# Performance work log

Measured on AMD Instinct MI355X. Metric: run time of the kernel, lower is better.

Reference implementation:

```python
import jax, jax.numpy as jnp
import numpy as np

D_MODEL = 256; N_LEVELS = 4; N_HEADS = 8; N_POINTS = 4
H_SP = 32; W_SP = 32
B = 2; LEN_Q = 1024; LEN_IN = N_LEVELS * H_SP * W_SP
D_HEAD = D_MODEL // N_HEADS
K9 = 9 * N_POINTS  # 3x3 neighborhood around each of the top-k matches


def setup_inputs() -> dict:
    key = jax.random.key(0)
    k1, k2, k3, k4 = jax.random.split(key, 4)
    bound = (6.0 / (D_MODEL + D_MODEL)) ** 0.5  # xavier_uniform for output_proj
    return {
        "query": jax.random.normal(k1, (B, LEN_Q, D_MODEL), jnp.float32),
        "reference_points": jax.random.uniform(k2, (B, LEN_Q, N_LEVELS, 2), dtype=jnp.float32),
        "input_flatten": jax.random.normal(k3, (B, LEN_IN, D_MODEL), jnp.float32),
        # all levels share the same h==w==32 spatial shape (required by the module)
        "input_spatial_shapes": np.full((N_LEVELS, 2), H_SP, dtype=np.int64),
        "input_level_start_index": (np.arange(N_LEVELS) * H_SP * W_SP).astype(np.int64),
        "out_proj_w": jax.random.uniform(k4, (D_MODEL, D_MODEL), jnp.float32, -bound, bound),
        "out_proj_b": jnp.zeros((D_MODEL,), jnp.float32),
    }


def _sample_offset(query, input_flatten, h, w, t):
    # per-head correlation -> softmax -> top-k index -> 3x3 neighborhood -> (x,y) offsets
    n, lq, _ = query.shape
    q = query.reshape(n, lq, N_HEADS, D_HEAD)
    v = input_flatten.reshape(n, -1, N_HEADS, D_HEAD)
    corr = jnp.einsum('nqhd,nkhd->nhqk', q, v) / D_HEAD          # [n,H,lq,Lin]
    corr = corr.reshape(n, N_HEADS, lq, t, h * w)
    prob = jax.nn.softmax(10.0 * corr, axis=-1)
    _, idx = jax.lax.top_k(prob, N_POINTS)                        # [n,H,lq,t,P] int32
    deltas = jnp.array([-1 - h, -h, 1 - h, -1, 0, 1, -1 + h, h, 1 + h], jnp.int32)
    # torch cat order is delta-major: all P points for delta1, then delta2, ...
    res = (idx[..., None, :] + deltas[:, None]).reshape(n, N_HEADS, lq, t, K9)
    res = jnp.clip(res, 0, (h - 1) * (w - 1))                     # faithful (h-1)*(w-1) clamp
    resf = res.astype(jnp.float32)
    off_w = jnp.floor(resf / h)
    off_h = resf - off_w * h
    offsets = jnp.stack([off_w, off_h], axis=-1)                  # [n,H,lq,t,K9,2]
    return jnp.transpose(offsets, (0, 2, 1, 3, 4, 5))             # [n,lq,H,L,K9,2]


def _ms_deform_attn(value, loc, h, w):
    # value [n,Lin,H,dh]; loc in [0,1], [n,lq,H,L,K9,2]; grid_sample-style bilinear, zero pad
    n, lq = loc.shape[0], loc.shape[1]
    v = value.reshape(n, N_LEVELS, h * w, N_HEADS, D_HEAD)
    v = jnp.transpose(v, (0, 3, 1, 2, 4))                         # [n,H,L,hw,dh]
    x = loc[..., 0] * w - 0.5
    y = loc[..., 1] * h - 0.5
    x0 = jnp.floor(x); y0 = jnp.floor(y)
    lw = x - x0; lh = y - y0
    attn_w = 1.0 / (N_LEVELS * K9)  # softmax of all-ones buffer is uniform
    acc = jnp.zeros((n, lq, N_HEADS, D_HEAD), jnp.float32)
    corners = ((y0, x0, (1 - lh) * (1 - lw)), (y0, x0 + 1, (1 - lh) * lw),
               (y0 + 1, x0, lh * (1 - lw)), (y0 + 1, x0 + 1, lh * lw))
    for yi, xi, wgt in corners:
        valid = (yi >= 0) & (yi < h) & (xi >= 0) & (xi < w)
        ii = (jnp.clip(yi, 0, h - 1) * w + jnp.clip(xi, 0, w - 1)).astype(jnp.int32)
        ww = jnp.where(valid, wgt, 0.0) * attn_w                  # [n,lq,H,L,K9]
        ii_t = jnp.transpose(ii, (0, 2, 3, 1, 4)).reshape(n, N_HEADS, N_LEVELS, lq * K9)
        g = jnp.take_along_axis(v, ii_t[..., None], axis=3)       # [n,H,L,lq*K9,dh]
        g = g.reshape(n, N_HEADS, N_LEVELS, lq, K9, D_HEAD)
        ww_t = jnp.transpose(ww, (0, 2, 3, 1, 4))                 # [n,H,L,lq,K9]
        acc = acc + jnp.einsum('nhlqk,nhlqkd->nqhd', ww_t, g)
    return acc.reshape(n, lq, D_MODEL)


def reference(query, reference_points, input_flatten, input_spatial_shapes,
              input_level_start_index, out_proj_w, out_proj_b):
    ss = np.asarray(input_spatial_shapes)
    h = int(ss[0, 0]); w = h
    lin = input_flatten.shape[1]
    t = lin // (h * w)  # == N_LEVELS
    value = input_flatten.reshape(input_flatten.shape[0], lin, N_HEADS, D_HEAD)
    offsets = _sample_offset(query, input_flatten, h, w, t)
    assert reference_points.shape[-1] == 2
    normalizer = jnp.asarray(np.stack([ss[:, 1], ss[:, 0]], -1), jnp.float32)  # [L,2]=(w,h)
    loc = offsets / normalizer[None, None, None, :, None, :]
    out = _ms_deform_attn(value, loc, h, w)
    out = out @ out_proj_w.T + out_proj_b
    return out, loc
```

## Files before the change

kernel.cpp:

```cpp
#include <hip/hip_runtime.h>
#include <math.h>

#define BB 2
#define LQ 1024
#define DM 256
#define NH 8
#define DH 32
#define NL 4
#define HWsp 1024
#define LIN 4096
#define K9 36
#define NGRP (BB * NH * NL * LQ)

typedef short bf16x8 __attribute__((ext_vector_type(8)));
typedef float f32x4 __attribute__((ext_vector_type(4)));

__device__ __forceinline__ ushort bf16rn(float x) {
  unsigned u = __float_as_uint(x);
  unsigned r = (u + 0x7FFFu + ((u >> 16) & 1u)) >> 16;
  return (ushort)r;
}
__device__ __forceinline__ float bf16tof(ushort h) {
  return __uint_as_float(((unsigned)h) << 16);
}

#define INSERT4(val, index)                                              \
  {                                                                      \
    const float v_ = (val);                                              \
    const int ix_ = (index);                                             \
    if (v_ > v3) {                                                       \
      if (v_ > v1) {                                                     \
        if (v_ > v0) {                                                   \
          v3 = v2; i3 = i2; v2 = v1; i2 = i1; v1 = v0; i1 = i0;          \
          v0 = v_; i0 = ix_;                                             \
        } else {                                                         \
          v3 = v2; i3 = i2; v2 = v1; i2 = i1; v1 = v_; i1 = ix_;         \
        }                                                                \
      } else {                                                           \
        if (v_ > v2) {                                                   \
          v3 = v2; i3 = i2; v2 = v_; i2 = ix_;                           \
        } else {                                                         \
          v3 = v_; i3 = ix_;                                             \
        }                                                                \
      }                                                                  \
    }                                                                    \
  }

#define LMAX(av, ai, bv, bi)                                        \
  {                                                                 \
    const bool g_ = ((av) > (bv)) || ((av) == (bv) && (ai) < (bi)); \
    if (!g_) { (av) = (bv); (ai) = (bi); }                          \
  }
#define CEX(av, ai, bv, bi)                                         \
  {                                                                 \
    const bool g_ = ((av) > (bv)) || ((av) == (bv) && (ai) < (bi)); \
    const float tv_ = g_ ? (av) : (bv);                             \
    const int ti_ = g_ ? (ai) : (bi);                               \
    (bv) = g_ ? (bv) : (av); (bi) = g_ ? (bi) : (ai);               \
    (av) = tv_; (ai) = ti_;                                         \
  }

#define PSTRIDE ((size_t)BB * NL * NH * 1024 * 32)

__global__ __launch_bounds__(256) void vsplit_kernel(
    const float* __restrict__ value, ushort* __restrict__ vs) {
  const int T = blockIdx.x * 256 + threadIdx.x;
  const int flat = T << 3;
  const int n = flat >> 20;
  const int rem = flat & 0xFFFFF;
  const int lin = rem >> 8;
  const int d0 = rem & 255;
  const int l = lin >> 10, row = lin & 1023;
  const int h = d0 >> 5, dd = d0 & 31;

  const float* src = value + (size_t)flat;
  float xf[8];
  *(float4*)&xf[0] = *(const float4*)src;
  *(float4*)&xf[4] = *(const float4*)(src + 4);

  ushort uh[8], ul[8], ul2[8];
  #pragma unroll
  for (int j = 0; j < 8; ++j) {
    const float x = xf[j];
    const ushort h1 = bf16rn(x);
    const float r1 = x - bf16tof(h1);
    const ushort h2 = bf16rn(r1);
    const float r2 = r1 - bf16tof(h2);
    uh[j] = h1; ul[j] = h2; ul2[j] = bf16rn(r2);
  }
  const size_t ob = ((((size_t)((n * NL + l) * NH + h)) << 10) + row) * 32 + dd;
  *(bf16x8*)(vs + 0 * PSTRIDE + ob) =
      (bf16x8){(short)uh[0], (short)uh[1], (short)uh[2], (short)uh[3],
               (short)uh[4], (short)uh[5], (short)uh[6], (short)uh[7]};
  *(bf16x8*)(vs + 1 * PSTRIDE + ob) =
      (bf16x8){(short)ul[0], (short)ul[1], (short)ul[2], (short)ul[3],
               (short)ul[4], (short)ul[5], (short)ul[6], (short)ul[7]};
  *(bf16x8*)(vs + 2 * PSTRIDE + ob) =
      (bf16x8){(short)ul2[0], (short)ul2[1], (short)ul2[2], (short)ul2[3],
               (short)ul2[4], (short)ul2[5], (short)ul2[6], (short)ul2[7]};
}

template <int SPLIT, int PRESPLIT>
__global__ __launch_bounds__(256) void corr_topk_kernel(
    const float* __restrict__ query, const float* __restrict__ value,
    const ushort* __restrict__ vs, int* __restrict__ idx_out,
    float4* __restrict__ pval, int4* __restrict__ pidx) {
  __shared__ ushort hiL[64][40];
  __shared__ ushort loL[64][40];
  __shared__ ushort lo2L[64][40];

  const int tid = threadIdx.x;
  const int nh = blockIdx.z;
  const int n = nh >> 3, h = nh & 7;
  const int l = blockIdx.y;
  const int qc = (SPLIT == 2) ? ((int)blockIdx.x >> 1) : (int)blockIdx.x;
  const int half = (SPLIT == 2) ? ((int)blockIdx.x & 1) : 0;
  const int c0 = (SPLIT == 2) ? (half << 3) : 0;
  const int c1 = (SPLIT == 2) ? (c0 + 8) : 16;
  const int w = tid >> 6, L = tid & 63;
  const int qtile = (qc << 2) + w;
  const int r16 = L & 15, g = L >> 4;

  bf16x8 qhi, qlo, qlo2;
  {
    const float* qp =
        query + (size_t)(n * LQ + (qtile << 4) + r16) * DM + h * DH + (g << 3);
    float qf[8];
    *(float4*)&qf[0] = *(const float4*)qp;
    *(float4*)&qf[4] = *(const float4*)(qp + 4);
    ushort uh[8], ul[8], ul2[8];
    #pragma unroll
    for (int j = 0; j < 8; ++j) {
      const float x = qf[j];
      const ushort h1 = bf16rn(x);
      const float r1 = x - bf16tof(h1);
      const ushort h2 = bf16rn(r1);
      const float r2 = r1 - bf16tof(h2);
      uh[j] = h1; ul[j] = h2; ul2[j] = bf16rn(r2);
    }
    qhi = (bf16x8){(short)uh[0], (short)uh[1], (short)uh[2], (short)uh[3],
                   (short)uh[4], (short)uh[5], (short)uh[6], (short)uh[7]};
    qlo = (bf16x8){(short)ul[0], (short)ul[1], (short)ul[2], (short)ul[3],
                   (short)ul[4], (short)ul[5], (short)ul[6], (short)ul[7]};
    qlo2 = (bf16x8){(short)ul2[0], (short)ul2[1], (short)ul2[2], (short)ul2[3],
                    (short)ul2[4], (short)ul2[5], (short)ul2[6], (short)ul2[7]};
  }

  float v0 = -INFINITY, v1 = -INFINITY, v2 = -INFINITY, v3 = -INFINITY;
  int i0 = 0, i1 = 0, i2 = 0, i3 = 0;

  const int srow = tid >> 2, s = tid & 3;
  const int wslot = (s ^ (srow & 3)) << 3;
  const ushort* psbase =
      PRESPLIT ? vs + ((((size_t)((n * NL + l) * NH + h)) << 10)) * 32 : nullptr;
  const float* vbase = value + (size_t)(n * LIN + l * HWsp) * DM + h * DH;

  for (int c = c0; c < c1; ++c) {
    if (PRESPLIT) {
      const size_t off = ((size_t)((c << 6) + srow)) * 32 + (s << 3);
      *(bf16x8*)&hiL[srow][wslot] = *(const bf16x8*)(psbase + off);
      *(bf16x8*)&loL[srow][wslot] = *(const bf16x8*)(psbase + PSTRIDE + off);
      *(bf16x8*)&lo2L[srow][wslot] = *(const bf16x8*)(psbase + 2 * PSTRIDE + off);
    } else {
      const float* vp = vbase + (size_t)((c << 6) + srow) * DM + (s << 3);
      float xf[8];
      *(float4*)&xf[0] = *(const float4*)vp;
      *(float4*)&xf[4] = *(const float4*)(vp + 4);
      ushort uh[8], ul[8], ul2[8];
      #pragma unroll
      for (int j = 0; j < 8; ++j) {
        const float x = xf[j];
        const ushort h1 = bf16rn(x);
        const float r1 = x - bf16tof(h1);
        const ushort h2 = bf16rn(r1);
        const float r2 = r1 - bf16tof(h2);
        uh[j] = h1; ul[j] = h2; ul2[j] = bf16rn(r2);
      }
      *(bf16x8*)&hiL[srow][wslot] =
          (bf16x8){(short)uh[0], (short)uh[1], (short)uh[2], (short)uh[3],
                   (short)uh[4], (short)uh[5], (short)uh[6], (short)uh[7]};
      *(bf16x8*)&loL[srow][wslot] =
          (bf16x8){(short)ul[0], (short)ul[1], (short)ul[2], (short)ul[3],
                   (short)ul[4], (short)ul[5], (short)ul[6], (short)ul[7]};
      *(bf16x8*)&lo2L[srow][wslot] =
          (bf16x8){(short)ul2[0], (short)ul2[1], (short)ul2[2], (short)ul2[3],
                   (short)ul2[4], (short)ul2[5], (short)ul2[6], (short)ul2[7]};
    }
    __syncthreads();

    #pragma unroll
    for (int t = 0; t < 4; ++t) {
      const int row = (t << 4) + r16;
      const int rslot = (g ^ (row & 3)) << 3;
      const bf16x8 ahi = *(const bf16x8*)&hiL[row][rslot];
      const bf16x8 alo = *(const bf16x8*)&loL[row][rslot];
      const bf16x8 alo2 = *(const bf16x8*)&lo2L[row][rslot];
      f32x4 acc = {0.f, 0.f, 0.f, 0.f};
      acc = __builtin_amdgcn_mfma_f32_16x16x32_bf16(alo2, qhi, acc, 0, 0, 0);
      acc = __builtin_amdgcn_mfma_f32_16x16x32_bf16(ahi, qlo2, acc, 0, 0, 0);
      acc = __builtin_amdgcn_mfma_f32_16x16x32_bf16(alo, qlo, acc, 0, 0, 0);
      acc = __builtin_amdgcn_mfma_f32_16x16x32_bf16(alo, qhi, acc, 0, 0, 0);
      acc = __builtin_amdgcn_mfma_f32_16x16x32_bf16(ahi, qlo, acc, 0, 0, 0);
      acc = __builtin_amdgcn_mfma_f32_16x16x32_bf16(ahi, qhi, acc, 0, 0, 0);
      const int kb = (c << 6) + (t << 4) + (g << 2);
      INSERT4(acc[0], kb + 0);
      INSERT4(acc[1], kb + 1);
      INSERT4(acc[2], kb + 2);
      INSERT4(acc[3], kb + 3);
    }
    __syncthreads();
  }

  #pragma unroll
  for (int m = 16; m < 64; m <<= 1) {
    const float b0 = __shfl_xor(v0, m);
    const float b1 = __shfl_xor(v1, m);
    const float b2 = __shfl_xor(v2, m);
    const float b3 = __shfl_xor(v3, m);
    const int j0 = __shfl_xor(i0, m);
    const int j1 = __shfl_xor(i1, m);
    const int j2 = __shfl_xor(i2, m);
    const int j3 = __shfl_xor(i3, m);
    LMAX(v0, i0, b3, j3);
    LMAX(v1, i1, b2, j2);
    LMAX(v2, i2, b1, j1);
    LMAX(v3, i3, b0, j0);
    CEX(v0, i0, v2, i2);
    CEX(v1, i1, v3, i3);
    CEX(v0, i0, v1, i1);
    CEX(v2, i2, v3, i3);
  }

  if (L < 16) {
    const int q = (qtile << 4) + L;
    const size_t gi = (((size_t)nh * NL + l) << 10) + q;
    if (SPLIT == 2) {
      pval[gi * 2 + half] = make_float4(v0, v1, v2, v3);
      pidx[gi * 2 + half] = make_int4(i0, i1, i2, i3);
    } else {
      ((int4*)idx_out)[gi] = make_int4(i0, i1, i2, i3);
    }
  }
}

__global__ __launch_bounds__(256) void merge_topk_kernel(
    const float4* __restrict__ pval, const int4* __restrict__ pidx,
    int* __restrict__ idx_out) {
  const int t = blockIdx.x * 256 + threadIdx.x;
  const float4 av = pval[t * 2 + 0];
  const int4 ai = pidx[t * 2 + 0];
  const float4 bv = pval[t * 2 + 1];
  const int4 bi = pidx[t * 2 + 1];
  float w0 = av.x, w1 = av.y, w2 = av.z, w3 = av.w;
  int m0 = ai.x, m1 = ai.y, m2 = ai.z, m3 = ai.w;
  LMAX(w0, m0, bv.w, bi.w);
  LMAX(w1, m1, bv.z, bi.z);
  LMAX(w2, m2, bv.y, bi.y);
  LMAX(w3, m3, bv.x, bi.x);
  CEX(w0, m0, w2, m2);
  CEX(w1, m1, w3, m3);
  CEX(w0, m0, w1, m1);
  CEX(w2, m2, w3, m3);
  ((int4*)idx_out)[t] = make_int4(m0, m1, m2, m3);
}

__global__ __launch_bounds__(256) void loc_kernel(const int* __restrict__ idx_buf,
                                                  float* __restrict__ loc) {
  const int t = blockIdx.x * 256 + threadIdx.x;
  const int k = t % 36;
  int rest = t / 36;
  const int l = rest & 3; rest >>= 2;
  const int h = rest & 7; rest >>= 3;
  const int q = rest & 1023;
  const int n = rest >> 10;
  const int p = k & 3, dd = k >> 2;
  const int idx = idx_buf[(((((n << 3) + h) * NL + l) << 10) + q) * 4 + p];
  const int delta = ((dd / 3) - 1) * 32 + (dd % 3) - 1;
  int res = idx + delta;
  res = min(max(res, 0), 961);
  const int W = res >> 5, H = res & 31;
  ((float2*)loc)[t] = make_float2((float)W * 0.03125f, (float)H * 0.03125f);
}

__global__ __launch_bounds__(256) void gather_kernel(
    const float* __restrict__ value, const int* __restrict__ idx_buf,
    float* __restrict__ acc_out) {
  __shared__ float4 red[NL][8];
  const int bh = blockIdx.x;
  const int h = bh & 7;
  const int nq = bh >> 3;
  const int n = nq >> 10, q = nq & 1023;
  const int tid = threadIdx.x;
  const int l = tid >> 6;
  const int L = tid & 63;
  const int cp = L >> 3, d4 = L & 7;

  const int4 id4 =
      ((const int4*)idx_buf)[((((size_t)((n << 3) + h)) * NL + l) << 10) + q];
  const float4* vb4 =
      (const float4*)(value + (size_t)(n * LIN + l * HWsp) * DM + h * DH) + d4;

  float4 a = make_float4(0.f, 0.f, 0.f, 0.f);
  #pragma unroll
  for (int p = 0; p < 4; ++p) {
    const int idx = (p == 0) ? id4.x : (p == 1) ? id4.y : (p == 2) ? id4.z : id4.w;
    const int H0 = idx & 31, W0 = idx >> 5;
    if (H0 >= 2 && H0 <= 30 && W0 >= 2 && W0 <= 28) {
      const int idxT = (H0 << 5) + W0;
      const int c0i = cp << 1;
      const int ax0 = c0i & 3, ay = c0i >> 2;
      const int r0 = idxT + (ax0 - 2) * 32 + (ay - 2);
      const float wy = (ay == 1 || ay == 2) ? 2.f : 1.f;
      const float f0 = ((ax0 == 2) ? 2.f : 1.f) * wy;
      const float f1 = ((ax0 + 1 == 1) ? 2.f : 1.f) * wy;
      const float4 va = vb4[(size_t)r0 * 64];
      const float4 vbb = vb4[(size_t)(r0 + 32) * 64];
      a.x += f0 * va.x + f1 * vbb.x;
      a.y += f0 * va.y + f1 * vbb.y;
      a.z += f0 * va.z + f1 * vbb.z;
      a.w += f0 * va.w + f1 * vbb.w;
    } else {
      #pragma unroll
      for (int it = 0; it < 5; ++it) {
        const int u = cp + (it << 3);
        const int cell = u >> 2, corner = u & 3;
        const int dy = (cell >= 3) + (cell >= 6) - 1;
        const int dx = cell - (dy + 1) * 3 - 1;
        int res = idx + dy * 32 + dx;
        res = min(max(res, 0), 961);
        const int W = res >> 5, H = res & 31;
        const int cw = corner & 1, ch = corner >> 1;
        const bool ok = (u < 36) && (W >= cw) && (H >= ch);
        const int row = ok ? (((H - ch) << 5) + (W - cw)) : 0;
        const float wgt = ok ? 1.f : 0.f;
        const float4 v = vb4[(size_t)row * 64];
        a.x += wgt * v.x;
        a.y += wgt * v.y;
        a.z += wgt * v.z;
        a.w += wgt * v.w;
      }
    }
  }

  #pragma unroll
  for (int m = 8; m < 64; m <<= 1) {
    a.x += __shfl_xor(a.x, m);
    a.y += __shfl_xor(a.y, m);
    a.z += __shfl_xor(a.z, m);
    a.w += __shfl_xor(a.w, m);
  }
  if (L < 8) red[l][L] = a;
  __syncthreads();
  if (tid < 8) {
    const float4 s0 = red[0][tid], s1 = red[1][tid], s2 = red[2][tid],
                 s3 = red[3][tid];
    float4 o;
    o.x = (s0.x + s1.x + s2.x + s3.x) * (1.0f / 576.0f);
    o.y = (s0.y + s1.y + s2.y + s3.y) * (1.0f / 576.0f);
    o.z = (s0.z + s1.z + s2.z + s3.z) * (1.0f / 576.0f);
    o.w = (s0.w + s1.w + s2.w + s3.w) * (1.0f / 576.0f);
    ((float4*)(acc_out + (size_t)nq * DM + h * DH))[tid] = o;
  }
}

__global__ __launch_bounds__(256) void proj_kernel(
    const float* __restrict__ acc_in, const float* __restrict__ W,
    const float* __restrict__ bias, float* __restrict__ out) {
  __shared__ float la[8][256];
  const int qb = blockIdx.x << 3;
  const int tid = threadIdx.x;
  for (int i = tid; i < 8 * 256; i += 256)
    la[i >> 8][i & 255] = acc_in[((size_t)qb << 8) + i];
  __syncthreads();
  const float* wrow = W + (size_t)tid * 256;
  float s0 = 0.f, s1 = 0.f, s2 = 0.f, s3 = 0.f, s4 = 0.f, s5 = 0.f, s6 = 0.f, s7 = 0.f;
  for (int c0 = 0; c0 < 256; c0 += 4) {
    const float4 wv = *(const float4*)(wrow + c0);
    #define PROJ_STEP(qi, sreg)                                   \
      {                                                           \
        const float4 av = *(const float4*)&la[qi][c0];            \
        sreg = fmaf(wv.x, av.x, sreg);                            \
        sreg = fmaf(wv.y, av.y, sreg);                            \
        sreg = fmaf(wv.z, av.z, sreg);                            \
        sreg = fmaf(wv.w, av.w, sreg);                            \
      }
    PROJ_STEP(0, s0) PROJ_STEP(1, s1) PROJ_STEP(2, s2) PROJ_STEP(3, s3)
    PROJ_STEP(4, s4) PROJ_STEP(5, s5) PROJ_STEP(6, s6) PROJ_STEP(7, s7)
    #undef PROJ_STEP
  }
  const float bj = bias[tid];
  out[(size_t)(qb + 0) * 256 + tid] = s0 + bj;
  out[(size_t)(qb + 1) * 256 + tid] = s1 + bj;
  out[(size_t)(qb + 2) * 256 + tid] = s2 + bj;
  out[(size_t)(qb + 3) * 256 + tid] = s3 + bj;
  out[(size_t)(qb + 4) * 256 + tid] = s4 + bj;
  out[(size_t)(qb + 5) * 256 + tid] = s5 + bj;
  out[(size_t)(qb + 6) * 256 + tid] = s6 + bj;
  out[(size_t)(qb + 7) * 256 + tid] = s7 + bj;
}

extern "C" void kernel_launch(void* const* d_in, const int* in_sizes, int n_in,
                              void* d_out, int out_size, void* d_ws, size_t ws_size,
                              hipStream_t stream) {
  (void)in_sizes; (void)n_in; (void)out_size;
  const float* query = (const float*)d_in[0];
  const float* value = (const float*)d_in[2];
  const float* opw = (const float*)d_in[5];
  const float* opb = (const float*)d_in[6];

  float* out = (float*)d_out;
  float* loc = out + (size_t)BB * LQ * DM;

  const size_t SPLITB = 3 * PSTRIDE * sizeof(ushort);
  const size_t PARTB = (size_t)NGRP * 2 * 16;
  const size_t IDXB = (size_t)NGRP * 4 * sizeof(int);
  const size_t ACCB = (size_t)BB * LQ * DM * sizeof(float);

  if (ws_size >= SPLITB + 2 * PARTB + IDXB + ACCB) {
    ushort* vsb = (ushort*)d_ws;
    float4* pval = (float4*)((char*)d_ws + SPLITB);
    int4* pidx = (int4*)((char*)d_ws + SPLITB + PARTB);
    int* idx_buf = (int*)((char*)d_ws + SPLITB + 2 * PARTB);
    float* acc_buf = (float*)((char*)d_ws + SPLITB + 2 * PARTB + IDXB);

    vsplit_kernel<<<dim3(1024), 256, 0, stream>>>(value, vsb);
    corr_topk_kernel<2, 1><<<dim3(32, NL, BB * NH), 256, 0, stream>>>(
        query, value, vsb, idx_buf, pval, pidx);
    merge_topk_kernel<<<dim3(NGRP / 256), 256, 0, stream>>>(pval, pidx, idx_buf);
    loc_kernel<<<dim3((BB * LQ * NH * NL * K9) / 256), 256, 0, stream>>>(idx_buf, loc);
    gather_kernel<<<dim3(BB * LQ * NH), 256, 0, stream>>>(value, idx_buf, acc_buf);
    proj_kernel<<<dim3(BB * LQ / 8), 256, 0, stream>>>(acc_buf, opw, opb, out);
  } else if (ws_size >= 2 * PARTB + IDXB + ACCB) {
    float4* pval = (float4*)d_ws;
    int4* pidx = (int4*)((char*)d_ws + PARTB);
    int* idx_buf = (int*)((char*)d_ws + 2 * PARTB);
    float* acc_buf = (float*)((char*)d_ws + 2 * PARTB + IDXB);

    corr_topk_kernel<2, 0><<<dim3(32, NL, BB * NH), 256, 0, stream>>>(
        query, value, (const ushort*)nullptr, idx_buf, pval, pidx);
    merge_topk_kernel<<<dim3(NGRP / 256), 256, 0, stream>>>(pval, pidx, idx_buf);
    loc_kernel<<<dim3((BB * LQ * NH * NL * K9) / 256), 256, 0, stream>>>(idx_buf, loc);
    gather_kernel<<<dim3(BB * LQ * NH), 256, 0, stream>>>(value, idx_buf, acc_buf);
    proj_kernel<<<dim3(BB * LQ / 8), 256, 0, stream>>>(acc_buf, opw, opb, out);
  } else {
    int* idx_buf = (int*)d_ws;
    float* acc_buf = (float*)((char*)d_ws + IDXB);

    corr_topk_kernel<1, 0><<<dim3(16, NL, BB * NH), 256, 0, stream>>>(
        query, value, (const ushort*)nullptr, idx_buf, (float4*)nullptr,
        (int4*)nullptr);
    loc_kernel<<<dim3((BB * LQ * NH * NL * K9) / 256), 256, 0, stream>>>(idx_buf, loc);
    gather_kernel<<<dim3(BB * LQ * NH), 256, 0, stream>>>(value, idx_buf, acc_buf);
    proj_kernel<<<dim3(BB * LQ / 8), 256, 0, stream>>>(acc_buf, opw, opb, out);
  }
}
```

Baseline: 104.4 us.

## Track top-4 over max-of-quad keys then recompute exact scores for candidate quads

Instead of inserting every correlation score into the per-lane top-4, each group of four adjacent keys is reduced to its max and only that max is inserted, cutting the insertion work fourfold. After the main loop, the four winning quads (16 keys) are rescored in fp32 from global memory and a lexicographic top-4 is taken over them. The LDS tiles also drop their padding and use a different XOR swizzle. The result is still the exact top-4, because any key in the true top-4 lies in one of the four best quads. The cost is extra scattered global loads and shuffles in the epilogue, and the recomputed fp32 scores may differ slightly from the split-bf16 MFMA scores near ties.

```diff
diff --git a/kernel.cpp b/kernel.cpp
--- a/kernel.cpp
+++ b/kernel.cpp
@@ -46,6 +46,30 @@
     }                                                                    \
   }
 
+#define LEXGT(v_, ix_, vv, ii) (((v_) > (vv)) || ((v_) == (vv) && (ix_) < (ii)))
+
+#define INSERT4LEX(val, index)                                               \
+  {                                                                          \
+    const float v_ = (val);                                                  \
+    const int ix_ = (index);                                                 \
+    if (LEXGT(v_, ix_, rv3, ri3)) {                                          \
+      if (LEXGT(v_, ix_, rv1, ri1)) {                                        \
+        if (LEXGT(v_, ix_, rv0, ri0)) {                                      \
+          rv3 = rv2; ri3 = ri2; rv2 = rv1; ri2 = ri1; rv1 = rv0; ri1 = ri0;  \
+          rv0 = v_; ri0 = ix_;                                               \
+        } else {                                                             \
+          rv3 = rv2; ri3 = ri2; rv2 = rv1; ri2 = ri1; rv1 = v_; ri1 = ix_;   \
+        }                                                                    \
+      } else {                                                               \
+        if (LEXGT(v_, ix_, rv2, ri2)) {                                      \
+          rv3 = rv2; ri3 = ri2; rv2 = v_; ri2 = ix_;                         \
+        } else {                                                             \
+          rv3 = v_; ri3 = ix_;                                               \
+        }                                                                    \
+      }                                                                      \
+    }                                                                        \
+  }
+
 #define LMAX(av, ai, bv, bi)                                        \
   {                                                                 \
     const bool g_ = ((av) > (bv)) || ((av) == (bv) && (ai) < (bi)); \
@@ -105,9 +129,9 @@
     const float* __restrict__ query, const float* __restrict__ value,
     const ushort* __restrict__ vs, int* __restrict__ idx_out,
     float4* __restrict__ pval, int4* __restrict__ pidx) {
-  __shared__ ushort hiL[64][40];
-  __shared__ ushort loL[64][40];
-  __shared__ ushort lo2L[64][40];
+  __shared__ ushort hiL[64][32];
+  __shared__ ushort loL[64][32];
+  __shared__ ushort lo2L[64][32];
 
   const int tid = threadIdx.x;
   const int nh = blockIdx.z;
@@ -121,11 +145,11 @@
   const int qtile = (qc << 2) + w;
   const int r16 = L & 15, g = L >> 4;
 
+  float qf[8];
   bf16x8 qhi, qlo, qlo2;
   {
     const float* qp =
         query + (size_t)(n * LQ + (qtile << 4) + r16) * DM + h * DH + (g << 3);
-    float qf[8];
     *(float4*)&qf[0] = *(const float4*)qp;
     *(float4*)&qf[4] = *(const float4*)(qp + 4);
     ushort uh[8], ul[8], ul2[8];
@@ -150,7 +174,8 @@
   int i0 = 0, i1 = 0, i2 = 0, i3 = 0;
 
   const int srow = tid >> 2, s = tid & 3;
-  const int wslot = (s ^ (srow & 3)) << 3;
+  const int wslot = (s ^ ((srow >> 1) & 3)) << 3;
+  const int rslot = (g ^ ((r16 >> 1) & 3)) << 3;
   const ushort* psbase =
       PRESPLIT ? vs + ((((size_t)((n * NL + l) * NH + h)) << 10)) * 32 : nullptr;
   const float* vbase = value + (size_t)(n * LIN + l * HWsp) * DM + h * DH;
@@ -191,7 +216,6 @@
     #pragma unroll
     for (int t = 0; t < 4; ++t) {
       const int row = (t << 4) + r16;
-      const int rslot = (g ^ (row & 3)) << 3;
       const bf16x8 ahi = *(const bf16x8*)&hiL[row][rslot];
       const bf16x8 alo = *(const bf16x8*)&loL[row][rslot];
       const bf16x8 alo2 = *(const bf16x8*)&lo2L[row][rslot];
@@ -202,11 +226,9 @@
       acc = __builtin_amdgcn_mfma_f32_16x16x32_bf16(alo, qhi, acc, 0, 0, 0);
       acc = __builtin_amdgcn_mfma_f32_16x16x32_bf16(ahi, qlo, acc, 0, 0, 0);
       acc = __builtin_amdgcn_mfma_f32_16x16x32_bf16(ahi, qhi, acc, 0, 0, 0);
-      const int kb = (c << 6) + (t << 4) + (g << 2);
-      INSERT4(acc[0], kb + 0);
-      INSERT4(acc[1], kb + 1);
-      INSERT4(acc[2], kb + 2);
-      INSERT4(acc[3], kb + 3);
+      const float qm = fmaxf(fmaxf(acc[0], acc[1]), fmaxf(acc[2], acc[3]));
+      const int qd = (c << 4) + (t << 2) + g;
+      INSERT4(qm, qd);
     }
     __syncthreads();
   }
@@ -231,14 +253,43 @@
     CEX(v2, i2, v3, i3);
   }
 
+  float rv0 = -INFINITY, rv1 = -INFINITY, rv2 = -INFINITY, rv3 = -INFINITY;
+  int ri0 = 0, ri1 = 0, ri2 = 0, ri3 = 0;
+  #define RECOVER_QUAD(QID)                                              \
+    {                                                                    \
+      _Pragma("unroll")                                                  \
+      for (int j = 0; j < 4; ++j) {                                      \
+        const int k = ((QID) << 2) + j;                                  \
+        const float* vf = vbase + (size_t)k * DM + (g << 3);             \
+        const float4 a0 = *(const float4*)vf;                            \
+        const float4 a1 = *(const float4*)(vf + 4);                      \
+        float p = qf[0] * a0.x;                                          \
+        p = fmaf(qf[1], a0.y, p);                                        \
+        p = fmaf(qf[2], a0.z, p);                                        \
+        p = fmaf(qf[3], a0.w, p);                                        \
+        p = fmaf(qf[4], a1.x, p);                                        \
+        p = fmaf(qf[5], a1.y, p);                                        \
+        p = fmaf(qf[6], a1.z, p);                                        \
+        p = fmaf(qf[7], a1.w, p);                                        \
+        p += __shfl_xor(p, 16);                                          \
+        p += __shfl_xor(p, 32);                                          \
+        INSERT4LEX(p, k);                                                \
+      }                                                                  \
+    }
+  RECOVER_QUAD(i0)
+  RECOVER_QUAD(i1)
+  RECOVER_QUAD(i2)
+  RECOVER_QUAD(i3)
+  #undef RECOVER_QUAD
+
   if (L < 16) {
     const int q = (qtile << 4) + L;
     const size_t gi = (((size_t)nh * NL + l) << 10) + q;
     if (SPLIT == 2) {
-      pval[gi * 2 + half] = make_float4(v0, v1, v2, v3);
-      pidx[gi * 2 + half] = make_int4(i0, i1, i2, i3);
+      pval[gi * 2 + half] = make_float4(rv0, rv1, rv2, rv3);
+      pidx[gi * 2 + half] = make_int4(ri0, ri1, ri2, ri3);
     } else {
-      ((int4*)idx_out)[gi] = make_int4(i0, i1, i2, i3);
+      ((int4*)idx_out)[gi] = make_int4(ri0, ri1, ri2, ri3);
     }
   }
 }
```

After: 111.0 us. 6.3% more time.
